# Kernel optimization log

Hardware: AMD Instinct MI355X
Metric: run time of the kernel (lower is better)

## Reference

```python
import jax, jax.numpy as jnp
import numpy as np

B, S, E, H = 2, 2048, 1024, 16
D = E // H  # head_dim = 64


def setup_inputs() -> dict:
    key = jax.random.key(0)
    k1, k2, k3 = jax.random.split(key, 3)
    scale_in = 1.0 / np.sqrt(E)
    return {
        "x": jax.random.normal(k1, (B, S, E), dtype=jnp.float32),
        "mask": jnp.ones((B, S), dtype=jnp.int32),
        "qkv_w": jax.random.normal(k2, (3 * E, E), dtype=jnp.float32) * scale_in,
        "qkv_b": jnp.zeros((3 * E,), dtype=jnp.float32),
        "proj_w": jax.random.normal(k3, (E, E), dtype=jnp.float32) * scale_in,
        "proj_b": jnp.zeros((E,), dtype=jnp.float32),
    }


def reference(x, mask, qkv_w, qkv_b, proj_w, proj_b):
    b, s, e = x.shape
    # fused QKV projection: torch Linear -> x @ W^T + b
    qkv = x @ qkv_w.T + qkv_b                      # [B,S,3E]
    qkv = qkv.reshape(b, s, 3, H, D).transpose(2, 0, 3, 1, 4)  # [3,B,H,S,D]
    q, k, v = qkv[0], qkv[1], qkv[2]
    scores = jnp.einsum("bhqd,bhkd->bhqk", q, k) / jnp.sqrt(jnp.float32(D))
    # mask [B,S] -> [B,1,1,S]; masked_fill(mask==0, -inf)
    m = mask[:, None, None, :]
    scores = jnp.where(m == 0, -jnp.inf, scores)
    attn = jax.nn.softmax(scores, axis=-1)
    attn = jnp.nan_to_num(attn, nan=0.0)           # fully-masked rows -> 0
    # dropout is identity in eval mode (deterministic reference)
    out = jnp.einsum("bhqk,bhkd->bhqd", attn, v)   # [B,H,S,D]
    out = out.transpose(0, 2, 1, 3).reshape(b, s, e)
    out = out @ proj_w.T + proj_b
    return out
```

## Files before the change

kernel.cpp:

```cpp
#include <hip/hip_runtime.h>
#include <hip/hip_bf16.h>

#define B_ 2
#define S_ 2048
#define E_ 1024
#define H_ 16
#define D_ 64

typedef __bf16 bf16x8 __attribute__((ext_vector_type(8)));
typedef __bf16 bf16x4 __attribute__((ext_vector_type(4)));
typedef float f32x4 __attribute__((ext_vector_type(4)));


__device__ __forceinline__ f32x4 mfma16(bf16x8 a, bf16x8 b, f32x4 c) {
    return __builtin_amdgcn_mfma_f32_16x16x32_bf16(a, b, c, 0, 0, 0);
}

__device__ __forceinline__ void gl_lds16(const __bf16* g, __bf16* l) {
    __builtin_amdgcn_global_load_lds(
        (const __attribute__((address_space(1))) unsigned int*)g,
        (__attribute__((address_space(3))) unsigned int*)l, 16, 0, 0);
}
__device__ __forceinline__ void gl_lds4(const int* g, int* l) {
    __builtin_amdgcn_global_load_lds(
        (const __attribute__((address_space(1))) unsigned int*)g,
        (__attribute__((address_space(3))) unsigned int*)l, 4, 0, 0);
}

__global__ __launch_bounds__(256) void convert_kernel(
        const float* __restrict__ x, const float* __restrict__ qkvw,
        const float* __restrict__ projw, __bf16* __restrict__ ws) {
    const long NX = 4194304, NW = 3145728;
    long i = (long)(blockIdx.x * 256 + threadIdx.x) * 4;
    const float* src; __bf16* dst; long off;
    if (i < NX)           { src = x;     dst = ws;           off = i; }
    else if (i < NX + NW) { src = qkvw;  dst = ws + NX;      off = i - NX; }
    else                  { src = projw; dst = ws + NX + NW; off = i - NX - NW; }
    float4 v = *(const float4*)(src + off);
    bf16x4 o = { (__bf16)v.x, (__bf16)v.y, (__bf16)v.z, (__bf16)v.w };
    *(bf16x4*)(dst + off) = o;
}

__device__ __forceinline__ void gemm_core(
        const __bf16* __restrict__ A, const __bf16* __restrict__ Bm,
        int rowT, int colT, int K,
        __bf16* AT, __bf16* BT, f32x4 acc[4][4]) {
    int tid = threadIdx.x;
    int wave = tid >> 6, lane = tid & 63;
    int quad = lane >> 4, lm = lane & 15;
    int wy = wave >> 1, wx = wave & 1;
    int srow = wave * 8 + (lane >> 3);
    int schunk = lane & 7;
    const __bf16* ap = A + (long)(rowT + srow) * K + schunk * 8;
    const __bf16* bp = Bm + (long)(colT + srow) * K + schunk * 8;
    for (int k0 = 0; k0 < K; k0 += 64) {
        __syncthreads();
        for (int i = 0; i < 4; i++) {
            gl_lds16(ap + (long)i * 32 * K + k0, AT + (i * 256 + wave * 64) * 8);
            gl_lds16(bp + (long)i * 32 * K + k0, BT + (i * 256 + wave * 64) * 8);
        }
        __syncthreads();
        for (int ks = 0; ks < 2; ks++) {
            bf16x8 af[4], bfr[4];
            for (int m = 0; m < 4; m++)
                af[m] = *(const bf16x8*)(AT + (wy * 64 + m * 16 + lm) * 64 + ks * 32 + quad * 8);
            for (int n = 0; n < 4; n++)
                bfr[n] = *(const bf16x8*)(BT + (wx * 64 + n * 16 + lm) * 64 + ks * 32 + quad * 8);
            for (int m = 0; m < 4; m++)
                for (int n = 0; n < 4; n++)
                    acc[m][n] = mfma16(af[m], bfr[n], acc[m][n]);
        }
    }
}

__device__ __forceinline__ void gemm_core_h(
        const __bf16* __restrict__ A, const __bf16* __restrict__ Bm,
        int rowT, int colT, int K,
        __bf16* AT, __bf16* BT, f32x4 acc[2][4]) {
    int tid = threadIdx.x;
    int wave = tid >> 6, lane = tid & 63;
    int quad = lane >> 4, lm = lane & 15;
    int srow = wave * 8 + (lane >> 3);
    int schunk = lane & 7;
    const __bf16* ap = A + (long)(rowT + srow) * K + schunk * 8;
    const __bf16* bp = Bm + (long)(colT + srow) * K + schunk * 8;
    for (int k0 = 0; k0 < K; k0 += 64) {
        __syncthreads();
        for (int i = 0; i < 4; i++)
            gl_lds16(ap + (long)i * 32 * K + k0, AT + (i * 256 + wave * 64) * 8);
        for (int i = 0; i < 2; i++)
            gl_lds16(bp + (long)i * 32 * K + k0, BT + (i * 256 + wave * 64) * 8);
        __syncthreads();
        for (int ks = 0; ks < 2; ks++) {
            bf16x8 af[2], bfr[4];
            for (int m = 0; m < 2; m++)
                af[m] = *(const bf16x8*)(AT + (wave * 32 + m * 16 + lm) * 64 + ks * 32 + quad * 8);
            for (int n = 0; n < 4; n++)
                bfr[n] = *(const bf16x8*)(BT + (n * 16 + lm) * 64 + ks * 32 + quad * 8);
            for (int m = 0; m < 2; m++)
                for (int n = 0; n < 4; n++)
                    acc[m][n] = mfma16(af[m], bfr[n], acc[m][n]);
        }
    }
}

#define C1 0.18033688011112043f

__global__ __launch_bounds__(256, 3) void qkv_gemm(
        const __bf16* __restrict__ xbf, const __bf16* __restrict__ wbf,
        const float* __restrict__ bias, __bf16* __restrict__ qk,
        __bf16* __restrict__ vt) {
    __shared__ __align__(16) __bf16 AT[128 * 64];
    __shared__ __align__(16) __bf16 BT[128 * 64];
    f32x4 acc[4][4] = {};
    int rowT = blockIdx.x * 128, colT = blockIdx.y * 128;
    gemm_core(xbf, wbf, rowT, colT, E_, AT, BT, acc);
    int wave = threadIdx.x >> 6, lane = threadIdx.x & 63;
    int quad = lane >> 4, lm = lane & 15;
    int wy = wave >> 1, wx = wave & 1;
    int which = colT >> 10;
    if (which < 2) {
        float sc = which ? 1.f : C1;
        for (int n = 0; n < 4; n++) {
            int col = colT + wx * 64 + n * 16 + lm;
            float bv = bias[col];
            int rem = col & 1023;
            int h = rem >> 6, d = rem & 63;
            for (int m = 0; m < 4; m++) {
                int rowb = rowT + wy * 64 + m * 16 + quad * 4;
                for (int r = 0; r < 4; r++) {
                    int row = rowb + r;
                    int b = row >> 11, s = row & 2047;
                    float v = (acc[m][n][r] + bv) * sc;
                    qk[(long)((which * B_ + b) * H_ + h) * (S_ * D_) + (long)s * D_ + d] = (__bf16)v;
                }
            }
        }
    } else {
        for (int n = 0; n < 4; n++) {
            int col = colT + wx * 64 + n * 16 + lm;
            float bv = bias[col];
            int mr = col & 1023;
            int h = mr >> 6, d = mr & 63;
            for (int m = 0; m < 4; m++) {
                int row = rowT + wy * 64 + m * 16 + quad * 4;
                int b = row >> 11, s = row & 2047;
                bf16x4 o = { (__bf16)(acc[m][n][0] + bv), (__bf16)(acc[m][n][1] + bv),
                             (__bf16)(acc[m][n][2] + bv), (__bf16)(acc[m][n][3] + bv) };
                *(bf16x4*)(vt + (long)((b * H_ + h) * D_ + d) * S_ + s) = o;
            }
        }
    }
}

__global__ __launch_bounds__(512, 2) void flash_attn(
        const __bf16* __restrict__ qk, const __bf16* __restrict__ vt,
        const int* __restrict__ mask, __bf16* __restrict__ attn) {
    int wave = threadIdx.x >> 6, lane = threadIdx.x & 63;
    int quad = lane >> 4, lm = lane & 15;
    int bh = blockIdx.x;
    int qb = blockIdx.y;
    int b = bh >> 4, h = bh & 15;
    const long BHSD = (long)B_ * H_ * S_ * D_;
    const __bf16* qp  = qk + (long)bh * (S_ * D_);
    const __bf16* kp  = qk + BHSD + (long)bh * (S_ * D_);
    const __bf16* vtp = vt + (long)bh * (D_ * S_);
    const int* mrow = mask + b * S_;

    __shared__ __align__(16) __bf16 Kl[2][128 * 64];
    __shared__ __align__(16) __bf16 Vl[2][64 * 128];
    __shared__ __align__(16) int    Ml[2][128];
    __shared__ __align__(16) __bf16 Plds[8][2][16][136];

    int q0[2];
    q0[0] = qb * 256 + wave * 32;
    q0[1] = q0[0] + 16;
    bf16x8 qa[2][2];
    for (int t = 0; t < 2; t++)
        for (int x = 0; x < 2; x++)
            qa[t][x] = *(const bf16x8*)(qp + (long)(q0[t] + lm) * D_ + x * 32 + quad * 8);

    f32x4 O[2][4] = {};
    f32x4 Ol[2] = {};
    bf16x8 ones8;
    for (int j = 0; j < 8; j++) ones8[j] = (__bf16)1.0f;
    const f32x4 zinit = {-32.f, -32.f, -32.f, -32.f};

    struct __align__(8) bfx4 { __hip_bfloat162 lo, hi; };

    int r8 = lane >> 3, c8 = lane & 7;
    int cs = c8 ^ r8;
    int xs = lm & 7;

    {
        #pragma unroll
        for (int j = 0; j < 2; j++) {
            int wp = wave * 2 + j;
            int krow = wp * 8 + r8;
            gl_lds16(kp + (long)krow * 64 + cs * 8, &Kl[0][wp * 512]);
            int vrow = wp * 4 + quad;
            int vcs = lm ^ (vrow & 15);
            gl_lds16(vtp + (long)vrow * S_ + vcs * 8, &Vl[0][wp * 512]);
        }
        if (wave == 0) {
            gl_lds4(mrow + lane, &Ml[0][0]);
            gl_lds4(mrow + 64 + lane, &Ml[0][64]);
        }
    }
    __syncthreads();

    for (int i = 0; i < 16; i++) {
        int bs = i & 1;
        if (i < 15) {
            int kb1 = (i + 1) * 128;
            #pragma unroll
            for (int j = 0; j < 2; j++) {
                int wp = wave * 2 + j;
                int krow = wp * 8 + r8;
                gl_lds16(kp + (long)(kb1 + krow) * 64 + cs * 8, &Kl[bs ^ 1][wp * 512]);
                int vrow = wp * 4 + quad;
                int vcs = lm ^ (vrow & 15);
                gl_lds16(vtp + (long)vrow * S_ + kb1 + vcs * 8, &Vl[bs ^ 1][wp * 512]);
            }
            if (wave == 0) {
                gl_lds4(mrow + kb1 + lane, &Ml[bs ^ 1][0]);
                gl_lds4(mrow + kb1 + 64 + lane, &Ml[bs ^ 1][64]);
            }
        }
        const __bf16* Kb = &Kl[bs][0];
        #pragma unroll
        for (int g = 0; g < 4; g++) {
            bf16x8 kf[2][2];
            int4 mq[2];
            #pragma unroll
            for (int j = 0; j < 2; j++) {
                int hh = g * 2 + j;
                int row = hh * 16 + lm;
                kf[j][0] = *(const bf16x8*)(Kb + row * 64 + ((quad ^ xs) << 3));
                kf[j][1] = *(const bf16x8*)(Kb + row * 64 + (((4 + quad) ^ xs) << 3));
                mq[j] = *(const int4*)(&Ml[bs][hh * 16 + quad * 4]);
            }
            f32x4 st[2][2];
            __builtin_amdgcn_s_setprio(1);
            #pragma unroll
            for (int j = 0; j < 2; j++)
                #pragma unroll
                for (int t = 0; t < 2; t++) {
                    f32x4 z = mfma16(kf[j][0], qa[t][0], zinit);
                    st[j][t] = mfma16(kf[j][1], qa[t][1], z);
                }
            __builtin_amdgcn_s_setprio(0);
            #pragma unroll
            for (int j = 0; j < 2; j++)
                #pragma unroll
                for (int t = 0; t < 2; t++) {
                    int hh = g * 2 + j;
                    float e0 = __builtin_amdgcn_exp2f(mq[j].x ? st[j][t][0] : -1e38f);
                    float e1 = __builtin_amdgcn_exp2f(mq[j].y ? st[j][t][1] : -1e38f);
                    float e2 = __builtin_amdgcn_exp2f(mq[j].z ? st[j][t][2] : -1e38f);
                    float e3 = __builtin_amdgcn_exp2f(mq[j].w ? st[j][t][3] : -1e38f);
                    bfx4 pk;
                    pk.lo = __float22bfloat162_rn(float2{e0, e1});
                    pk.hi = __float22bfloat162_rn(float2{e2, e3});
                    *(bfx4*)(&Plds[wave][t][lm][hh * 16 + quad * 4]) = pk;
                }
        }
        const __bf16* Vb = &Vl[bs][0];
        #pragma unroll
        for (int x = 0; x < 4; x++) {
            bf16x8 vf[4];
            #pragma unroll
            for (int c = 0; c < 4; c++) {
                int row = c * 16 + lm;
                vf[c] = *(const bf16x8*)(Vb + row * 128 + (((x * 4 + quad) ^ lm) << 3));
            }
            bf16x8 pa[2];
            #pragma unroll
            for (int t = 0; t < 2; t++)
                pa[t] = *(const bf16x8*)(&Plds[wave][t][lm][x * 32 + quad * 8]);
            __builtin_amdgcn_s_setprio(1);
            #pragma unroll
            for (int t = 0; t < 2; t++) {
                #pragma unroll
                for (int c = 0; c < 4; c++)
                    O[t][c] = mfma16(pa[t], vf[c], O[t][c]);
                Ol[t] = mfma16(pa[t], ones8, Ol[t]);
            }
            __builtin_amdgcn_s_setprio(0);
        }
        __syncthreads();
    }

    for (int t = 0; t < 2; t++)
        for (int r = 0; r < 4; r++) {
            float lb = Ol[t][r];
            float inv = lb > 0.f ? 1.f / lb : 0.f;
            int s = q0[t] + quad * 4 + r;
            for (int c = 0; c < 4; c++) {
                int e = h * 64 + c * 16 + lm;
                attn[(long)(b * S_ + s) * E_ + e] = (__bf16)(O[t][c][r] * inv);
            }
        }
}

__global__ __launch_bounds__(256, 2) void proj_gemm(
        const __bf16* __restrict__ abf, const __bf16* __restrict__ wbf,
        const float* __restrict__ bias, float* __restrict__ out) {
    __shared__ __align__(16) __bf16 AT[128 * 64];
    __shared__ __align__(16) __bf16 BT[64 * 64];
    f32x4 acc[2][4] = {};
    int rowT = blockIdx.x * 128, colT = blockIdx.y * 64;
    gemm_core_h(abf, wbf, rowT, colT, E_, AT, BT, acc);
    int wave = threadIdx.x >> 6, lane = threadIdx.x & 63;
    int quad = lane >> 4, lm = lane & 15;
    for (int n = 0; n < 4; n++) {
        int col = colT + n * 16 + lm;
        float bv = bias[col];
        for (int m = 0; m < 2; m++) {
            int rowb = rowT + wave * 32 + m * 16 + quad * 4;
            for (int r = 0; r < 4; r++) {
                int row = rowb + r;
                out[(long)row * E_ + col] = acc[m][n][r] + bv;
            }
        }
    }
}

extern "C" void kernel_launch(void* const* d_in, const int* in_sizes, int n_in,
                              void* d_out, int out_size, void* d_ws, size_t ws_size,
                              hipStream_t stream) {
    const float* x      = (const float*)d_in[0];
    const int*   mask   = (const int*)d_in[1];
    const float* qkv_w  = (const float*)d_in[2];
    const float* qkv_b  = (const float*)d_in[3];
    const float* proj_w = (const float*)d_in[4];
    const float* proj_b = (const float*)d_in[5];
    float* out = (float*)d_out;
    __bf16* ws = (__bf16*)d_ws;

    __bf16* x_bf     = ws;
    __bf16* qkvw_bf  = ws + 4194304;
    __bf16* projw_bf = ws + 7340032;
    __bf16* qk_bf    = ws + 8388608;
    __bf16* vt_bf    = ws + 16777216;
    __bf16* attn_bf  = ws + 20971520;

    convert_kernel<<<8192, 256, 0, stream>>>(x, qkv_w, proj_w, ws);
    qkv_gemm<<<dim3(32, 24), 256, 0, stream>>>(x_bf, qkvw_bf, qkv_b, qk_bf, vt_bf);
    flash_attn<<<dim3(32, 8), 512, 0, stream>>>(qk_bf, vt_bf, mask, attn_bf);
    proj_gemm<<<dim3(32, 16), 256, 0, stream>>>(attn_bf, projw_bf, proj_b, out);
}
```

Measured before the change: 186.7 us.

## Keep softmax probabilities in registers by permuting V^T layout, fold mask into MFMA init

```diff
diff --git a/kernel.cpp b/kernel.cpp
--- a/kernel.cpp
+++ b/kernel.cpp
@@ -145,9 +145,10 @@
             for (int m = 0; m < 4; m++) {
                 int row = rowT + wy * 64 + m * 16 + quad * 4;
                 int b = row >> 11, s = row & 2047;
+                int j = (s & ~31) | (((s >> 2) & 3) << 3) | (((s >> 4) & 1) << 2);
                 bf16x4 o = { (__bf16)(acc[m][n][0] + bv), (__bf16)(acc[m][n][1] + bv),
                              (__bf16)(acc[m][n][2] + bv), (__bf16)(acc[m][n][3] + bv) };
-                *(bf16x4*)(vt + (long)((b * H_ + h) * D_ + d) * S_ + s) = o;
+                *(bf16x4*)(vt + (long)((b * H_ + h) * D_ + d) * S_ + j) = o;
             }
         }
     }
@@ -170,7 +171,6 @@
     __shared__ __align__(16) __bf16 Kl[2][128 * 64];
     __shared__ __align__(16) __bf16 Vl[2][64 * 128];
     __shared__ __align__(16) int    Ml[2][128];
-    __shared__ __align__(16) __bf16 Plds[8][2][16][136];
 
     int q0[2];
     q0[0] = qb * 256 + wave * 32;
@@ -184,9 +184,6 @@
     f32x4 Ol[2] = {};
     bf16x8 ones8;
     for (int j = 0; j < 8; j++) ones8[j] = (__bf16)1.0f;
-    const f32x4 zinit = {-32.f, -32.f, -32.f, -32.f};
-
-    struct __align__(8) bfx4 { __hip_bfloat162 lo, hi; };
 
     int r8 = lane >> 3, c8 = lane & 7;
     int cs = c8 ^ r8;
@@ -228,17 +225,22 @@
             }
         }
         const __bf16* Kb = &Kl[bs][0];
+        unsigned int pw[8][2][2];
         #pragma unroll
         for (int g = 0; g < 4; g++) {
             bf16x8 kf[2][2];
-            int4 mq[2];
+            f32x4 zsel[2];
             #pragma unroll
             for (int j = 0; j < 2; j++) {
                 int hh = g * 2 + j;
                 int row = hh * 16 + lm;
                 kf[j][0] = *(const bf16x8*)(Kb + row * 64 + ((quad ^ xs) << 3));
                 kf[j][1] = *(const bf16x8*)(Kb + row * 64 + (((4 + quad) ^ xs) << 3));
-                mq[j] = *(const int4*)(&Ml[bs][hh * 16 + quad * 4]);
+                int4 mq = *(const int4*)(&Ml[bs][hh * 16 + quad * 4]);
+                zsel[j][0] = mq.x ? -32.f : -1e38f;
+                zsel[j][1] = mq.y ? -32.f : -1e38f;
+                zsel[j][2] = mq.z ? -32.f : -1e38f;
+                zsel[j][3] = mq.w ? -32.f : -1e38f;
             }
             f32x4 st[2][2];
             __builtin_amdgcn_s_setprio(1);
@@ -246,7 +248,7 @@
             for (int j = 0; j < 2; j++)
                 #pragma unroll
                 for (int t = 0; t < 2; t++) {
-                    f32x4 z = mfma16(kf[j][0], qa[t][0], zinit);
+                    f32x4 z = mfma16(kf[j][0], qa[t][0], zsel[j]);
                     st[j][t] = mfma16(kf[j][1], qa[t][1], z);
                 }
             __builtin_amdgcn_s_setprio(0);
@@ -255,14 +257,15 @@
                 #pragma unroll
                 for (int t = 0; t < 2; t++) {
                     int hh = g * 2 + j;
-                    float e0 = __builtin_amdgcn_exp2f(mq[j].x ? st[j][t][0] : -1e38f);
-                    float e1 = __builtin_amdgcn_exp2f(mq[j].y ? st[j][t][1] : -1e38f);
-                    float e2 = __builtin_amdgcn_exp2f(mq[j].z ? st[j][t][2] : -1e38f);
-                    float e3 = __builtin_amdgcn_exp2f(mq[j].w ? st[j][t][3] : -1e38f);
-                    bfx4 pk;
-                    pk.lo = __float22bfloat162_rn(float2{e0, e1});
-                    pk.hi = __float22bfloat162_rn(float2{e2, e3});
-                    *(bfx4*)(&Plds[wave][t][lm][hh * 16 + quad * 4]) = pk;
+                    float e0 = __builtin_amdgcn_exp2f(st[j][t][0]);
+                    float e1 = __builtin_amdgcn_exp2f(st[j][t][1]);
+                    float e2 = __builtin_amdgcn_exp2f(st[j][t][2]);
+                    float e3 = __builtin_amdgcn_exp2f(st[j][t][3]);
+                    union { __hip_bfloat162 b; unsigned int u; } plo, phi;
+                    plo.b = __float22bfloat162_rn(float2{e0, e1});
+                    phi.b = __float22bfloat162_rn(float2{e2, e3});
+                    pw[hh][t][0] = plo.u;
+                    pw[hh][t][1] = phi.u;
                 }
         }
         const __bf16* Vb = &Vl[bs][0];
@@ -276,8 +279,14 @@
             }
             bf16x8 pa[2];
             #pragma unroll
-            for (int t = 0; t < 2; t++)
-                pa[t] = *(const bf16x8*)(&Plds[wave][t][lm][x * 32 + quad * 8]);
+            for (int t = 0; t < 2; t++) {
+                union { unsigned int u[4]; bf16x8 v; } pu;
+                pu.u[0] = pw[2 * x][t][0];
+                pu.u[1] = pw[2 * x][t][1];
+                pu.u[2] = pw[2 * x + 1][t][0];
+                pu.u[3] = pw[2 * x + 1][t][1];
+                pa[t] = pu.v;
+            }
             __builtin_amdgcn_s_setprio(1);
             #pragma unroll
             for (int t = 0; t < 2; t++) {
```

Result: no change. 187.5 us (+0.4%).
